# Kernel optimization log

Hardware: AMD Instinct MI355X
Metric: run time of the kernel (lower is better)

Reference implementation:

```python
import jax, jax.numpy as jnp
import numpy as np
import math

DIM = 1280
NUM_HEADS = 16
HEAD_DIM = DIM // NUM_HEADS  # 80
SEQ = 3072


def setup_inputs() -> dict:
    key = jax.random.key(0)
    ks = jax.random.split(key, 6)
    hidden_states = jax.random.normal(ks[0], (SEQ, DIM), dtype=jnp.float32)
    cu_seqlens = jnp.array([0, 768, 1536, 2304, 3072], dtype=jnp.int32)
    # rotary angles for half the head dim, as produced by the vision rotary embedding
    rotary_pos_emb = jax.random.uniform(ks[1], (SEQ, HEAD_DIM // 2), dtype=jnp.float32) * 10.0
    qkv_w = jax.random.normal(ks[2], (3 * DIM, DIM), dtype=jnp.float32) * (1.0 / math.sqrt(DIM))
    qkv_b = jax.random.normal(ks[3], (3 * DIM,), dtype=jnp.float32) * 0.02
    proj_w = jax.random.normal(ks[4], (DIM, DIM), dtype=jnp.float32) * (1.0 / math.sqrt(DIM))
    proj_b = jax.random.normal(ks[5], (DIM,), dtype=jnp.float32) * 0.02
    return {"hidden_states": hidden_states, "cu_seqlens": cu_seqlens,
            "rotary_pos_emb": rotary_pos_emb, "qkv_w": qkv_w, "qkv_b": qkv_b,
            "proj_w": proj_w, "proj_b": proj_b}


def _rotate_half(x):
    half = x.shape[-1] // 2
    return jnp.concatenate([-x[..., half:], x[..., :half]], axis=-1)


def _apply_rotary(t, rotary_pos_emb):
    # t: [seq, heads, head_dim]; rotary_pos_emb: [seq, head_dim//2]
    emb = jnp.concatenate([rotary_pos_emb, rotary_pos_emb], axis=-1)  # [seq, head_dim]
    cos = jnp.cos(emb)[:, None, :]
    sin = jnp.sin(emb)[:, None, :]
    return t * cos + _rotate_half(t) * sin


def reference(hidden_states, cu_seqlens, rotary_pos_emb, qkv_w, qkv_b, proj_w, proj_b):
    seq = hidden_states.shape[0]
    qkv = hidden_states @ qkv_w.T + qkv_b                       # [seq, 3*dim]
    qkv = qkv.reshape(seq, 3, NUM_HEADS, HEAD_DIM)
    q, k, v = qkv[:, 0], qkv[:, 1], qkv[:, 2]                   # [seq, h, d]
    q = _apply_rotary(q, rotary_pos_emb)
    k = _apply_rotary(k, rotary_pos_emb)

    # block-diagonal mask: token i attends to token j iff same segment
    seg = jnp.searchsorted(cu_seqlens[1:], jnp.arange(seq), side='right')
    same = seg[:, None] == seg[None, :]                         # [seq, seq] bool
    neg = jnp.finfo(q.dtype).min
    add_mask = jnp.where(same, jnp.float32(0), neg).astype(q.dtype)

    scale = 1.0 / math.sqrt(HEAD_DIM)
    scores = jnp.einsum('nhd,mhd->hnm', q, k) * scale           # [h, seq, seq]
    scores = scores + add_mask[None, :, :]
    attn = jax.nn.softmax(scores.astype(jnp.float32), axis=-1).astype(q.dtype)
    out = jnp.einsum('hnm,mhd->nhd', attn, v).reshape(seq, DIM)
    return out @ proj_w.T + proj_b
```

## Files before the change

kernel.cpp:

```cpp
#include <hip/hip_runtime.h>

#define SEQ 3072
#define NH 16
#define HD 80
#define SEGLEN 768

typedef unsigned short u16;
typedef unsigned int u32;
typedef float f32x4 __attribute__((ext_vector_type(4)));
typedef __bf16 bf16x8 __attribute__((ext_vector_type(8)));
typedef short short8 __attribute__((ext_vector_type(8)));
typedef u16 u16x4 __attribute__((ext_vector_type(4)));

#define WAITV(N) asm volatile("s_waitcnt vmcnt(" #N ")" ::: "memory")

__device__ __forceinline__ u16 f2bf(float f) {
  u32 u = __builtin_bit_cast(u32, f);
  u32 r = u + 0x7fffu + ((u >> 16) & 1u);
  return (u16)(r >> 16);
}
__device__ __forceinline__ float bf2f(u16 x) {
  u32 u = ((u32)x) << 16;
  return __builtin_bit_cast(float, u);
}

__device__ __forceinline__ f32x4 mfma16(short8 a, short8 b, f32x4 c) {
  return __builtin_amdgcn_mfma_f32_16x16x32_bf16(
      __builtin_bit_cast(bf16x8, a), __builtin_bit_cast(bf16x8, b), c, 0, 0, 0);
}

__device__ __forceinline__ void gload_lds16(const u16* g, u16* l) {
  __builtin_amdgcn_global_load_lds(
      (const __attribute__((address_space(1))) u32*)(g),
      (__attribute__((address_space(3))) u32*)(l), 16, 0, 0);
}

__global__ __launch_bounds__(256) void cvt3(const float* __restrict__ a, u16* __restrict__ ao, int na,
                                            const float* __restrict__ b, u16* __restrict__ bo, int nb,
                                            const float* __restrict__ c, u16* __restrict__ co, int nc) {
  int i = blockIdx.x * 256 + threadIdx.x;
  const float* src;
  u16* dst;
  int n;
  if (i < na) { src = a; dst = ao; n = i; }
  else if (i < na + nb) { src = b; dst = bo; n = i - na; }
  else if (i < na + nb + nc) { src = c; dst = co; n = i - na - nb; }
  else return;
  f32x4 v = ((const f32x4*)src)[n];
  u16x4 o;
  o[0] = f2bf(v[0]); o[1] = f2bf(v[1]); o[2] = f2bf(v[2]); o[3] = f2bf(v[3]);
  ((u16x4*)dst)[n] = o;
}

__global__ __launch_bounds__(512) void gemm_8p(
    const u16* __restrict__ A, const u16* __restrict__ B,
    const float* __restrict__ bias, u16* __restrict__ C,
    int M, int N, int K) {
  __shared__ u16 LB[2 * 4 * 8192];
  char* lds = (char*)LB;
  const int tid = threadIdx.x, lane = tid & 63, w = tid >> 6;
  const int wm = w >> 2, wn = w & 3;
  const int lr = lane & 15, lg = lane >> 4;
  const int br = blockIdx.y * 256, bc = blockIdx.x * 256;
  const int NT = K >> 6;

  f32x4 acc[8][4];
#pragma unroll
  for (int m = 0; m < 8; ++m)
#pragma unroll
    for (int n = 0; n < 4; ++n) acc[m][n] = (f32x4){0.f, 0.f, 0.f, 0.f};

  const int r0 = tid >> 2, s0 = tid & 3;
  const int r1 = r0 + 128;
  const u16* sA0 = A + (br + r0) * (size_t)K + (((s0 - (r0 >> 1)) & 3) << 3);
  const u16* sA1 = A + (br + r1) * (size_t)K + (((s0 - (r1 >> 1)) & 3) << 3);
  const u16* sB0 = B + (bc + r0) * (size_t)K + (((s0 - (r0 >> 1)) & 3) << 3);
  const u16* sB1 = B + (bc + r1) * (size_t)K + (((s0 - (r1 >> 1)) & 3) << 3);
  const int d0 = tid * 16, d1 = (tid + 512) * 16;

  auto stg = [&](const u16* g0, const u16* g1, int kcol, int buf, int half) {
    char* hb = lds + buf * 65536 + half * 16384;
    gload_lds16(g0 + kcol, (u16*)(hb + d0));
    gload_lds16(g1 + kcol, (u16*)(hb + d1));
  };

  int aoff[8], boff[4];
#pragma unroll
  for (int m = 0; m < 8; ++m) {
    int row = wm * 128 + m * 16 + lr;
    aoff[m] = row * 64 + ((lg + (row >> 1)) & 3) * 16;
  }
#pragma unroll
  for (int n = 0; n < 4; ++n) {
    int row = wn * 64 + n * 16 + lr;
    boff[n] = row * 64 + ((lg + (row >> 1)) & 3) * 16;
  }

  stg(sA0, sA1, 0, 0, 0);
  stg(sA0, sA1, 32, 0, 1);
  stg(sB0, sB1, 0, 0, 2);
  stg(sB0, sB1, 32, 0, 3);
  stg(sA0, sA1, 64, 1, 0);
  stg(sB0, sB1, 64, 1, 2);
  WAITV(4);
  __builtin_amdgcn_s_barrier();

  for (int t = 0; t < NT; ++t) {
    const int p = t & 1;
    const char* Ab = lds + p * 65536;
    const char* Bb = Ab + 32768;
#pragma unroll
    for (int q = 0; q < 4; ++q) {
      const char* Ah = Ab + (q >> 1) * 16384;
      const char* Bh = Bb + (q >> 1) * 16384;
      short8 af[8], bf0, bf1;
#pragma unroll
      for (int m = 0; m < 8; ++m) af[m] = *(const short8*)(Ah + aoff[m]);
      const int nb = (q & 1) * 2;
      bf0 = *(const short8*)(Bh + boff[nb]);
      bf1 = *(const short8*)(Bh + boff[nb + 1]);
      if (q == 0) { if (t + 1 < NT) stg(sA0, sA1, (t + 1) * 64 + 32, p ^ 1, 1); }
      else if (q == 1) { if (t + 1 < NT) stg(sB0, sB1, (t + 1) * 64 + 32, p ^ 1, 3); }
      else if (q == 2) { if (t + 2 < NT) stg(sA0, sA1, (t + 2) * 64, p, 0); }
      else { if (t + 2 < NT) stg(sB0, sB1, (t + 2) * 64, p, 2); }
      __builtin_amdgcn_s_setprio(1);
#pragma unroll
      for (int m = 0; m < 8; ++m) {
        acc[m][nb] = mfma16(af[m], bf0, acc[m][nb]);
        acc[m][nb + 1] = mfma16(af[m], bf1, acc[m][nb + 1]);
      }
      __builtin_amdgcn_s_setprio(0);
      if (q == 3) {
        if (t == NT - 2) WAITV(0);
        else if (t < NT - 2) WAITV(4);
      }
      __builtin_amdgcn_s_barrier();
    }
  }

#pragma unroll
  for (int n = 0; n < 4; ++n) {
    int col = bc + wn * 64 + n * 16 + lr;
    float bv = bias[col];
#pragma unroll
    for (int m = 0; m < 8; ++m) {
      int rowb = br + wm * 128 + m * 16 + lg * 4;
#pragma unroll
      for (int r = 0; r < 4; ++r)
        C[(size_t)(rowb + r) * N + col] = f2bf(acc[m][n][r] + bv);
    }
  }
}

template <int OUT_BF16, int WM, int WN>
__global__ __launch_bounds__(256) void gemm_p3(
    const u16* __restrict__ A, const u16* __restrict__ B,
    const float* __restrict__ bias, void* __restrict__ Cv,
    int M, int N, int K) {
  constexpr int BM = 32 * WM, BN = 32 * WN;
  constexpr int ROWS = BM + BN;
  constexpr int L = ROWS / 64;
  static_assert(L == 3, "tuned for L=3");
  __shared__ u16 LB[3][ROWS * 32];
  const int tid = threadIdx.x, lane = tid & 63, w = tid >> 6;
  const int wr = (w >> 1) * (WM * 16), wc = (w & 1) * (WN * 16);
  const int lr = lane & 15, lg = lane >> 4;
  const int gy = gridDim.y;
  const int fc = blockIdx.x * gy + blockIdx.y;
  const int cpx = (gridDim.x * gy) >> 3;
  const int f = (fc & 7) * cpx + (fc >> 3);
  const int bx = f / gy, by = f % gy;
  const int br = by * BM, bc = bx * BN;
  const int NT = K >> 5;

  f32x4 acc[WM][WN];
#pragma unroll
  for (int m = 0; m < WM; ++m)
#pragma unroll
    for (int n = 0; n < WN; ++n) acc[m][n] = (f32x4){0.f, 0.f, 0.f, 0.f};

  const u16* sp[L];
#pragma unroll
  for (int c = 0; c < L; ++c) {
    int ch = c * 256 + tid;
    int row = ch >> 2, sl = ch & 3;
    int scol = ((sl - (row >> 1)) & 3) << 3;
    sp[c] = (row < BM ? A + (br + row) * (size_t)K
                      : B + (bc + row - BM) * (size_t)K) + scol;
  }
  auto stage = [&](int t, int buf) {
#pragma unroll
    for (int c = 0; c < L; ++c)
      gload_lds16(sp[c] + t * 32, &LB[buf][(c * 256 + tid) * 8]);
  };

  int aoff[WM], boff[WN];
#pragma unroll
  for (int m = 0; m < WM; ++m) {
    int row = wr + m * 16 + lr;
    aoff[m] = row * 64 + ((lg + (row >> 1)) & 3) * 16;
  }
#pragma unroll
  for (int n = 0; n < WN; ++n) {
    int row = BM + wc + n * 16 + lr;
    boff[n] = row * 64 + ((lg + (row >> 1)) & 3) * 16;
  }

  auto step = [&](int t, int buf, bool issue, int wn) {
    if (issue) stage(t + 2, (t + 2) % 3);
    const char* base = (const char*)&LB[buf][0];
    short8 af[WM], bf[WN];
#pragma unroll
    for (int m = 0; m < WM; ++m) af[m] = *(const short8*)(base + aoff[m]);
#pragma unroll
    for (int n = 0; n < WN; ++n) bf[n] = *(const short8*)(base + boff[n]);
#pragma unroll
    for (int m = 0; m < WM; ++m)
#pragma unroll
      for (int n = 0; n < WN; ++n) acc[m][n] = mfma16(af[m], bf[n], acc[m][n]);
    if (wn == 3) WAITV(3);
    else if (wn == 0) WAITV(0);
    if (wn >= 0) __builtin_amdgcn_s_barrier();
  };

  stage(0, 0);
  stage(1, 1);
  WAITV(3);
  __builtin_amdgcn_s_barrier();

  int t = 0;
  for (; t + 3 <= NT - 2; t += 3) {
    step(t + 0, 0, true, 3);
    step(t + 1, 1, true, 3);
    step(t + 2, 2, true, 3);
  }
  step(NT - 4, 0, true, 3);
  step(NT - 3, 1, true, 3);
  step(NT - 2, 2, false, 0);
  step(NT - 1, 0, false, -1);

#pragma unroll
  for (int n = 0; n < WN; ++n) {
    int col = bc + wc + n * 16 + lr;
    float bv = bias[col];
#pragma unroll
    for (int m = 0; m < WM; ++m) {
      int rowb = br + wr + m * 16 + lg * 4;
#pragma unroll
      for (int r = 0; r < 4; ++r) {
        float v = acc[m][n][r] + bv;
        if (OUT_BF16)
          ((u16*)Cv)[(rowb + r) * N + col] = f2bf(v);
        else
          ((float*)Cv)[(rowb + r) * N + col] = v;
      }
    }
  }
}

__global__ __launch_bounds__(256) void prep_kern(
    const u16* __restrict__ qkvb, const float* __restrict__ rpe,
    u16* __restrict__ qb, u16* __restrict__ kb, u16* __restrict__ vt) {
  const int bid = blockIdx.x, tid = threadIdx.x;
  if (bid < 3072) {
    const float QSCL = 0.16129841769519493f;
    const u16* row = qkvb + bid * 3840;
#pragma unroll
    for (int it = 0; it < 5; ++it) {
      int idx = it * 256 + tid;
      int d = idx % 80;
      float e = rpe[bid * 40 + (d % 40)];
      float s, c;
      sincosf(e, &s, &c);
      float qv = bf2f(row[idx]);
      float qo = (d < 40) ? -bf2f(row[idx + 40]) : bf2f(row[idx - 40]);
      float kv = bf2f(row[1280 + idx]);
      float ko = (d < 40) ? -bf2f(row[1280 + idx + 40]) : bf2f(row[1280 + idx - 40]);
      int o = bid * 1280 + idx;
      qb[o] = f2bf((qv * c + qo * s) * QSCL);
      kb[o] = f2bf(kv * c + ko * s);
    }
  } else {
    __shared__ u16 tile[64 * 84];
    const int vb = bid - 3072;
    const int s0 = (vb % 48) * 64, h = vb / 48;
#pragma unroll
    for (int c = 0; c < 20; ++c) {
      int ch = c * 256 + tid;
      int r = ch / 80, d = ch % 80;
      tile[r * 84 + d] = qkvb[(s0 + r) * 3840 + 2560 + h * 80 + d];
    }
    __syncthreads();
#pragma unroll
    for (int c = 0; c < 20; ++c) {
      int ch = c * 256 + tid;
      int d = ch >> 6, r = ch & 63;
      vt[(h * 96 + d) * 3072 + s0 + r] = tile[r * 84 + d];
    }
    if (tid < 64) vt[(h * 96 + 80) * 3072 + s0 + tid] = 0x3F80;
  }
}

__global__ __launch_bounds__(256) void attn_kern(
    const u16* __restrict__ qb, const u16* __restrict__ kb,
    const u16* __restrict__ vt, u16* __restrict__ ob) {
  __shared__ u16 SH[26176];
  char* shb = (char*)SH;
  const int tid = threadIdx.x, lane = tid & 63, w = tid >> 6;
  const int lr = lane & 15, lg = lane >> 4;
  const int xcd = blockIdx.x & 7, t = blockIdx.x >> 3;
  const int qt = t % 12, shhi = t / 12;
  const int sh = xcd + shhi * 8;
  const int seg = sh >> 4, h = sh & 15;
  const int qrow = seg * SEGLEN + qt * 64 + w * 16 + lr;

  short8 qf[3];
#pragma unroll
  for (int kk = 0; kk < 3; ++kk) {
    int d = kk * 32 + lg * 8;
    if (d < 80)
      qf[kk] = *(const short8*)(qb + qrow * 1280 + h * 80 + d);
    else
      qf[kk] = (short8){0, 0, 0, 0, 0, 0, 0, 0};
  }
  f32x4 oa[6];
#pragma unroll
  for (int n = 0; n < 6; ++n) oa[n] = (f32x4){0.f, 0.f, 0.f, 0.f};
  float mrow[4] = {-1e30f, -1e30f, -1e30f, -1e30f};

  const u16* kseg = kb + seg * SEGLEN * 1280 + h * 80;
  const u16* vseg = vt + (h * 96) * 3072 + seg * SEGLEN;

  auto stageK = [&](int buf, int it) {
    const u16* kbase = kseg + it * 64 * 1280;
#pragma unroll
    for (int c = 0; c < 4; ++c) {
      int ch = c * 256 + tid;
      int kv = ch >> 4, sl = ch & 15;
      gload_lds16(kbase + kv * 1280 + ((sl ^ (kv & 7)) << 3),
                  (u16*)(shb + buf * 16384 + ch * 16));
    }
  };
  auto stageV = [&](int it) {
    const u16* vbase = vseg + it * 64;
#pragma unroll
    for (int c = 0; c < 3; ++c) {
      int ch = c * 256 + tid;
      if (ch < 648) {
        int d = ch >> 3, sl = ch & 7;
        gload_lds16(vbase + d * 3072 + ((sl ^ (d & 7)) << 3),
                    (u16*)(shb + 32768 + ch * 16));
      }
    }
  };

  stageK(0, 0);
  stageV(0);
  __syncthreads();
  int cur = 0;
  char* PsW = shb + 43136 + w * 2304;
  const char* Vc = shb + 32768;

  for (int it = 0; it < 12; ++it) {
    if (it > 0) stageV(it);
    if (it < 11) stageK(cur ^ 1, it + 1);
    const char* Kc = shb + cur * 16384;
    f32x4 sf[4];
#pragma unroll
    for (int n = 0; n < 4; ++n) {
      sf[n] = (f32x4){0.f, 0.f, 0.f, 0.f};
#pragma unroll
      for (int kk = 0; kk < 3; ++kk) {
        int row = n * 16 + lr;
        int X = kk * 64 + lg * 16;
        short8 kf = *(const short8*)(Kc + row * 256 + (X ^ ((row & 7) << 4)));
        __builtin_amdgcn_s_setprio(1);
        sf[n] = mfma16(qf[kk], kf, sf[n]);
        __builtin_amdgcn_s_setprio(0);
      }
    }
    float mx[4];
#pragma unroll
    for (int r = 0; r < 4; ++r) {
      float a = fmaxf(fmaxf(sf[0][r], sf[1][r]), fmaxf(sf[2][r], sf[3][r]));
      a = fmaxf(a, __shfl_xor(a, 1, 16));
      a = fmaxf(a, __shfl_xor(a, 2, 16));
      a = fmaxf(a, __shfl_xor(a, 4, 16));
      a = fmaxf(a, __shfl_xor(a, 8, 16));
      mx[r] = a;
    }
    float need = fmaxf(fmaxf(mx[0] - mrow[0], mx[1] - mrow[1]),
                       fmaxf(mx[2] - mrow[2], mx[3] - mrow[3]));
    if (!__all(need <= 8.0f)) {
#pragma unroll
      for (int r = 0; r < 4; ++r) {
        float m = fmaxf(mrow[r], mx[r]);
        float f = exp2f(mrow[r] - m);
        mrow[r] = m;
#pragma unroll
        for (int n = 0; n < 6; ++n) oa[n][r] *= f;
      }
    }
#pragma unroll
    for (int r = 0; r < 4; ++r) {
      float p0 = exp2f(sf[0][r] - mrow[r]), p1 = exp2f(sf[1][r] - mrow[r]);
      float p2 = exp2f(sf[2][r] - mrow[r]), p3 = exp2f(sf[3][r] - mrow[r]);
      int offb = (lg * 4 + r) * 144 + lr * 2;
      *(u16*)(PsW + offb + ((lg ^ 0) << 5)) = f2bf(p0);
      *(u16*)(PsW + offb + ((lg ^ 1) << 5)) = f2bf(p1);
      *(u16*)(PsW + offb + ((lg ^ 2) << 5)) = f2bf(p2);
      *(u16*)(PsW + offb + ((lg ^ 3) << 5)) = f2bf(p3);
    }
    __syncthreads();
#pragma unroll
    for (int kt = 0; kt < 2; ++kt) {
      short8 pf = *(const short8*)(PsW + lr * 144 +
                                   ((((kt << 1) + (lg >> 1)) ^ (lr >> 2)) << 5) +
                                   ((lg & 1) << 4));
#pragma unroll
      for (int n = 0; n < 6; ++n) {
        int dcol = n * 16 + lr;
        int X = kt * 64 + lg * 16;
        short8 vf = *(const short8*)(Vc + dcol * 128 + (X ^ ((dcol & 7) << 4)));
        __builtin_amdgcn_s_setprio(1);
        oa[n] = mfma16(pf, vf, oa[n]);
        __builtin_amdgcn_s_setprio(0);
      }
    }
    __syncthreads();
    cur ^= 1;
  }
#pragma unroll
  for (int r = 0; r < 4; ++r) {
    float lsum = __shfl(oa[5][r], lane & 48, 64);
    float linv = 1.0f / lsum;
    int orow = seg * SEGLEN + qt * 64 + w * 16 + lg * 4 + r;
#pragma unroll
    for (int n = 0; n < 5; ++n)
      ob[orow * 1280 + h * 80 + n * 16 + lr] = f2bf(oa[n][r] * linv);
  }
}

extern "C" void kernel_launch(void* const* d_in, const int* in_sizes, int n_in,
                              void* d_out, int out_size, void* d_ws, size_t ws_size,
                              hipStream_t stream) {
  const float* hs = (const float*)d_in[0];
  const float* rpe = (const float*)d_in[2];
  const float* qkvw = (const float*)d_in[3];
  const float* qkv_b = (const float*)d_in[4];
  const float* pw = (const float*)d_in[5];
  const float* pb = (const float*)d_in[6];
  float* out = (float*)d_out;

  char* ws = (char*)d_ws;
  u16* hsb = (u16*)(ws);
  u16* wqkvb = (u16*)(ws + 7864320);
  u16* wprojb = (u16*)(ws + 17694720);
  u16* qkvb = (u16*)(ws + 20971520);
  u16* vt = (u16*)(ws + 44564480);
  u16* qb = hsb;
  u16* kb = wqkvb;
  u16* aob = qkvb;

  cvt3<<<10240, 256, 0, stream>>>(hs, hsb, 983040, qkvw, wqkvb, 1228800, pw, wprojb, 409600);
  gemm_8p<<<dim3(15, 12), 512, 0, stream>>>(hsb, wqkvb, qkv_b, qkvb, 3072, 3840, 1280);
  prep_kern<<<3840, 256, 0, stream>>>(qkvb, rpe, qb, kb, vt);
  attn_kern<<<768, 256, 0, stream>>>(qb, kb, vt, aob);
  gemm_p3<0, 2, 4><<<dim3(10, 48), 256, 0, stream>>>(aob, wprojb, pb, out, 3072, 1280, 1280);
}
```

Before: 132.0 us.

## Shrink QKV GEMM M-tile to 192 rows for better CU fill

The QKV projection GEMM tile changes from 256x256 to 192x256, so the grid grows from 180 to 240 workgroups and fills the 256 CUs more evenly. The LDS staging is reworked so each K-step loads A and B halves for the next buffer together, replacing the four-phase two-ahead prefetch with a simpler double-buffered one-ahead pipeline with a barrier per half-step. The cost is less reuse per tile and possibly less latency hiding from the shallower prefetch.

```diff
diff --git a/kernel.cpp b/kernel.cpp
--- a/kernel.cpp
+++ b/kernel.cpp
@@ -52,42 +52,50 @@
   ((u16x4*)dst)[n] = o;
 }
 
-__global__ __launch_bounds__(512) void gemm_8p(
+__global__ __launch_bounds__(512) void gemm_192(
     const u16* __restrict__ A, const u16* __restrict__ B,
     const float* __restrict__ bias, u16* __restrict__ C,
     int M, int N, int K) {
-  __shared__ u16 LB[2 * 4 * 8192];
+  __shared__ u16 LB[2 * 28672];
   char* lds = (char*)LB;
   const int tid = threadIdx.x, lane = tid & 63, w = tid >> 6;
   const int wm = w >> 2, wn = w & 3;
   const int lr = lane & 15, lg = lane >> 4;
-  const int br = blockIdx.y * 256, bc = blockIdx.x * 256;
+  const int br = blockIdx.y * 192, bc = blockIdx.x * 256;
   const int NT = K >> 6;
 
-  f32x4 acc[8][4];
-#pragma unroll
-  for (int m = 0; m < 8; ++m)
+  f32x4 acc[6][4];
+#pragma unroll
+  for (int m = 0; m < 6; ++m)
 #pragma unroll
     for (int n = 0; n < 4; ++n) acc[m][n] = (f32x4){0.f, 0.f, 0.f, 0.f};
 
-  const int r0 = tid >> 2, s0 = tid & 3;
-  const int r1 = r0 + 128;
-  const u16* sA0 = A + (br + r0) * (size_t)K + (((s0 - (r0 >> 1)) & 3) << 3);
-  const u16* sA1 = A + (br + r1) * (size_t)K + (((s0 - (r1 >> 1)) & 3) << 3);
-  const u16* sB0 = B + (bc + r0) * (size_t)K + (((s0 - (r0 >> 1)) & 3) << 3);
-  const u16* sB1 = B + (bc + r1) * (size_t)K + (((s0 - (r1 >> 1)) & 3) << 3);
-  const int d0 = tid * 16, d1 = (tid + 512) * 16;
-
-  auto stg = [&](const u16* g0, const u16* g1, int kcol, int buf, int half) {
-    char* hb = lds + buf * 65536 + half * 16384;
-    gload_lds16(g0 + kcol, (u16*)(hb + d0));
-    gload_lds16(g1 + kcol, (u16*)(hb + d1));
-  };
-
-  int aoff[8], boff[4];
-#pragma unroll
-  for (int m = 0; m < 8; ++m) {
-    int row = wm * 128 + m * 16 + lr;
+  const int chA0 = w * 96 + lane, chA1 = w * 96 + 64 + lane;
+  const int chB0 = w * 128 + lane, chB1 = w * 128 + 64 + lane;
+  auto srcptr = [&](const u16* Mx, int base, int ch, int Kd) {
+    int row = ch >> 2, sl = ch & 3;
+    return Mx + (size_t)(base + row) * Kd + (((sl - (row >> 1)) & 3) << 3);
+  };
+  const u16* sA0 = srcptr(A, br, chA0, K);
+  const u16* sA1 = srcptr(A, br, chA1 < 768 ? chA1 : chA0, K);
+  const u16* sB0 = srcptr(B, bc, chB0, K);
+  const u16* sB1 = srcptr(B, bc, chB1, K);
+
+  auto stgA = [&](int kcol, int buf, int half) {
+    char* hb = lds + buf * 57344 + half * 12288;
+    gload_lds16(sA0 + kcol, (u16*)(hb + chA0 * 16));
+    if (lane < 32) gload_lds16(sA1 + kcol, (u16*)(hb + chA1 * 16));
+  };
+  auto stgB = [&](int kcol, int buf, int half) {
+    char* hb = lds + buf * 57344 + 24576 + half * 16384;
+    gload_lds16(sB0 + kcol, (u16*)(hb + chB0 * 16));
+    gload_lds16(sB1 + kcol, (u16*)(hb + chB1 * 16));
+  };
+
+  int aoff[6], boff[4];
+#pragma unroll
+  for (int m = 0; m < 6; ++m) {
+    int row = wm * 96 + m * 16 + lr;
     aoff[m] = row * 64 + ((lg + (row >> 1)) & 3) * 16;
   }
 #pragma unroll
@@ -96,45 +104,40 @@
     boff[n] = row * 64 + ((lg + (row >> 1)) & 3) * 16;
   }
 
-  stg(sA0, sA1, 0, 0, 0);
-  stg(sA0, sA1, 32, 0, 1);
-  stg(sB0, sB1, 0, 0, 2);
-  stg(sB0, sB1, 32, 0, 3);
-  stg(sA0, sA1, 64, 1, 0);
-  stg(sB0, sB1, 64, 1, 2);
+  stgA(0, 0, 0); stgB(0, 0, 0);
+  stgA(32, 0, 1); stgB(32, 0, 1);
   WAITV(4);
   __builtin_amdgcn_s_barrier();
 
   for (int t = 0; t < NT; ++t) {
     const int p = t & 1;
-    const char* Ab = lds + p * 65536;
-    const char* Bb = Ab + 32768;
-#pragma unroll
-    for (int q = 0; q < 4; ++q) {
-      const char* Ah = Ab + (q >> 1) * 16384;
-      const char* Bh = Bb + (q >> 1) * 16384;
-      short8 af[8], bf0, bf1;
-#pragma unroll
-      for (int m = 0; m < 8; ++m) af[m] = *(const short8*)(Ah + aoff[m]);
-      const int nb = (q & 1) * 2;
-      bf0 = *(const short8*)(Bh + boff[nb]);
-      bf1 = *(const short8*)(Bh + boff[nb + 1]);
-      if (q == 0) { if (t + 1 < NT) stg(sA0, sA1, (t + 1) * 64 + 32, p ^ 1, 1); }
-      else if (q == 1) { if (t + 1 < NT) stg(sB0, sB1, (t + 1) * 64 + 32, p ^ 1, 3); }
-      else if (q == 2) { if (t + 2 < NT) stg(sA0, sA1, (t + 2) * 64, p, 0); }
-      else { if (t + 2 < NT) stg(sB0, sB1, (t + 2) * 64, p, 2); }
+    const char* bufb = lds + p * 57344;
+#pragma unroll
+    for (int q = 0; q < 2; ++q) {
+      const char* Ah = bufb + q * 12288;
+      const char* Bh = bufb + 24576 + q * 16384;
+      short8 af[6], bf[4];
+#pragma unroll
+      for (int m = 0; m < 6; ++m) af[m] = *(const short8*)(Ah + aoff[m]);
+#pragma unroll
+      for (int n = 0; n < 4; ++n) bf[n] = *(const short8*)(Bh + boff[n]);
+      if (t + 1 < NT) {
+        stgA((t + 1) * 64 + q * 32, p ^ 1, q);
+        stgB((t + 1) * 64 + q * 32, p ^ 1, q);
+      }
       __builtin_amdgcn_s_setprio(1);
 #pragma unroll
-      for (int m = 0; m < 8; ++m) {
-        acc[m][nb] = mfma16(af[m], bf0, acc[m][nb]);
-        acc[m][nb + 1] = mfma16(af[m], bf1, acc[m][nb + 1]);
-      }
+      for (int m = 0; m < 6; ++m)
+#pragma unroll
+        for (int n = 0; n < 4; ++n) acc[m][n] = mfma16(af[m], bf[n], acc[m][n]);
       __builtin_amdgcn_s_setprio(0);
-      if (q == 3) {
-        if (t == NT - 2) WAITV(0);
-        else if (t < NT - 2) WAITV(4);
-      }
-      __builtin_amdgcn_s_barrier();
+      if (t + 1 < NT) {
+        WAITV(4);
+        __builtin_amdgcn_s_barrier();
+      } else if (q == 0) {
+        WAITV(0);
+        __builtin_amdgcn_s_barrier();
+      }
     }
   }
 
@@ -143,8 +146,8 @@
     int col = bc + wn * 64 + n * 16 + lr;
     float bv = bias[col];
 #pragma unroll
-    for (int m = 0; m < 8; ++m) {
-      int rowb = br + wm * 128 + m * 16 + lg * 4;
+    for (int m = 0; m < 6; ++m) {
+      int rowb = br + wm * 96 + m * 16 + lg * 4;
 #pragma unroll
       for (int r = 0; r < 4; ++r)
         C[(size_t)(rowb + r) * N + col] = f2bf(acc[m][n][r] + bv);
@@ -463,7 +466,7 @@
   u16* aob = qkvb;
 
   cvt3<<<10240, 256, 0, stream>>>(hs, hsb, 983040, qkvw, wqkvb, 1228800, pw, wprojb, 409600);
-  gemm_8p<<<dim3(15, 12), 512, 0, stream>>>(hsb, wqkvb, qkv_b, qkvb, 3072, 3840, 1280);
+  gemm_192<<<dim3(15, 16), 512, 0, stream>>>(hsb, wqkvb, qkv_b, qkvb, 3072, 3840, 1280);
   prep_kern<<<3840, 256, 0, stream>>>(qkvb, rpe, qb, kb, vt);
   attn_kern<<<768, 256, 0, stream>>>(qb, kb, vt, aob);
   gemm_p3<0, 2, 4><<<dim3(10, 48), 256, 0, stream>>>(aob, wprojb, pb, out, 3072, 1280, 1280);
```

Result: faster. 127.0 us (-3.8%).
